# Performance work log

Measured on AMD Instinct MI355X. Metric: run time of the kernel, lower is better.

## Reference

```python
import jax, jax.numpy as jnp
import numpy as np

CH = 64
SCALE = 2
GROUPS = 4
K = 3
GN_GROUPS = min(CH // 8, 8)  # = 8
EPS_GN = 1e-5
EPS_COS = 1e-8


def setup_inputs() -> dict:
    key = jax.random.key(0)
    ks = jax.random.split(key, 4)
    B, H, W = 8, 256, 256
    OC = 2 * GROUPS
    lap = jnp.array([[0., -1., 0.], [-1., 4., -1.], [0., -1., 0.]], dtype=jnp.float32)
    hp_weight = jnp.tile(lap[None, None], (CH, 1, 1, 1))  # depthwise high-pass kernel
    return {
        "x": jax.random.normal(ks[0], (B, CH, H, W), dtype=jnp.float32),
        "gn_gamma": jnp.ones((CH,), jnp.float32),
        "gn_beta": jnp.zeros((CH,), jnp.float32),
        "hp_weight": hp_weight,
        "dir_w": jax.random.normal(ks[1], (OC, K * K - 1), jnp.float32) * 0.001,
        "dir_b": jnp.zeros((OC,), jnp.float32),
        "mag_w": jax.random.normal(ks[2], (OC, CH), jnp.float32) * 0.02,
        "mag_b": jnp.zeros((OC,), jnp.float32),
        "hfg_w": jax.random.normal(ks[3], (OC, CH), jnp.float32) * 0.02,
        "hfg_b": jnp.zeros((OC,), jnp.float32),
    }


def group_norm(x, gamma, beta, g, eps=EPS_GN):
    B, C, H, W = x.shape
    xr = x.reshape(B, g, -1)
    mu = xr.mean(-1, keepdims=True)
    var = xr.var(-1, keepdims=True)
    xn = ((xr - mu) * jax.lax.rsqrt(var + eps)).reshape(B, C, H, W)
    return xn * gamma[None, :, None, None] + beta[None, :, None, None]


def dw_conv3(x, w):
    # depthwise 3x3, padding=1, no bias
    return jax.lax.conv_general_dilated(
        x, w, window_strides=(1, 1), padding=((1, 1), (1, 1)),
        dimension_numbers=("NCHW", "OIHW", "NCHW"), feature_group_count=x.shape[1])


def avg_pool(x, s):
    B, C, H, W = x.shape
    return x.reshape(B, C, H // s, s, W // s, s).mean(axis=(3, 5))


def direction_feat(x, k=K):
    # cosine similarity (over channels) of center pixel vs each of k*k neighbors, center dropped
    B, C, H, W = x.shape
    p = k // 2
    xp = jnp.pad(x, ((0, 0), (0, 0), (p, p), (p, p)))
    patches = jnp.stack([xp[:, :, i:i + H, j:j + W]
                         for i in range(k) for j in range(k)], axis=2)  # [B,C,k2,H,W]
    center = patches[:, :, k * k // 2:k * k // 2 + 1]  # [B,C,1,H,W]
    dot = (center * patches).sum(axis=1)               # [B,k2,H,W]
    n1 = jnp.sqrt((center * center).sum(axis=1))       # [B,1,H,W]
    n2 = jnp.sqrt((patches * patches).sum(axis=1))     # [B,k2,H,W]
    sim = dot / (jnp.maximum(n1, EPS_COS) * jnp.maximum(n2, EPS_COS))
    c = k * k // 2
    return jnp.concatenate([sim[:, :c], sim[:, c + 1:]], axis=1)  # [B,k2-1,H,W]


def conv1x1(w, b, x):
    return jnp.einsum("oc,bchw->bohw", w, x) + b[None, :, None, None]


def grid_sample_border(x, grid):
    # x: [N,C,H,W]; grid: [N,Hg,Wg,2] in [-1,1]; bilinear, align_corners=False, padding_mode='border'
    N, C, H, W = x.shape
    gx, gy = grid[..., 0], grid[..., 1]
    ix = jnp.clip(((gx + 1.0) * W - 1.0) * 0.5, 0.0, W - 1.0)
    iy = jnp.clip(((gy + 1.0) * H - 1.0) * 0.5, 0.0, H - 1.0)
    x0 = jnp.floor(ix); y0 = jnp.floor(iy)
    wx = (ix - x0)[..., None]; wy = (iy - y0)[..., None]
    x0i = jnp.clip(x0.astype(jnp.int32), 0, W - 1)
    y0i = jnp.clip(y0.astype(jnp.int32), 0, H - 1)
    x1i = jnp.clip(x0i + 1, 0, W - 1)
    y1i = jnp.clip(y0i + 1, 0, H - 1)
    img = x.transpose(0, 2, 3, 1)  # [N,H,W,C]
    b = jnp.arange(N)[:, None, None]
    v00 = img[b, y0i, x0i]; v01 = img[b, y0i, x1i]
    v10 = img[b, y1i, x0i]; v11 = img[b, y1i, x1i]
    out = (v00 * (1 - wx) * (1 - wy) + v01 * wx * (1 - wy)
           + v10 * (1 - wx) * wy + v11 * wx * wy)
    return out.transpose(0, 3, 1, 2)  # [N,C,Hg,Wg]


def reference(x, gn_gamma, gn_beta, hp_weight, dir_w, dir_b, mag_w, mag_b, hfg_w, hfg_b):
    B, C, H, W = x.shape
    xn = group_norm(x, gn_gamma, gn_beta, GN_GROUPS)
    hf = dw_conv3(xn, hp_weight)
    xl = avg_pool(xn, SCALE)
    hfl = avg_pool(hf, SCALE)
    df = direction_feat(xl)
    gate = jax.nn.sigmoid(conv1x1(mag_w, mag_b, xl) + conv1x1(hfg_w, hfg_b, hfl))
    offset = conv1x1(dir_w, dir_b, df) * gate  # [B, 2*GROUPS, Hl, Wl]
    Hl, Wl = H // SCALE, W // SCALE
    off = offset.reshape(B, 2, GROUPS, Hl, Wl)
    cy = jnp.arange(Hl, dtype=x.dtype) * SCALE + SCALE / 2.0  # high-res pixel centers
    cx = jnp.arange(Wl, dtype=x.dtype) * SCALE + SCALE / 2.0
    gx = (cx[None, None, None, :] + off[:, 0]) * (2.0 / W) - 1.0  # [B,G,Hl,Wl]
    gy = (cy[None, None, :, None] + off[:, 1]) * (2.0 / H) - 1.0
    grid = jnp.stack([gx, gy], axis=-1).reshape(B * GROUPS, Hl, Wl, 2)
    xg = x.reshape(B * GROUPS, C // GROUPS, H, W)
    out = grid_sample_border(xg, grid)
    return out.reshape(B, C, Hl, Wl)
```

## Files before the change

### kernel.cpp

```cpp
#include <hip/hip_runtime.h>
#include <hip/hip_bf16.h>
#include <math.h>

#define B_ 8
#define C_ 64
#define H_ 256
#define W_ 256
#define HL_ 128
#define WL_ 128
#define GN_G 8
#define CPG 8
#define GRP 4
#define OC_ 8
#define GROUP_ELEMS (CPG * H_ * W_)

#define TILE_H 16
#define XROWS 34
#define EOW 132

__global__ __launch_bounds__(256) void k2_fused(const float* __restrict__ x,
                                                const float* __restrict__ hpw,
                                                float* __restrict__ px,
                                                float* __restrict__ pL,
                                                float* __restrict__ partials) {
  __shared__ float E[XROWS][EOW];
  __shared__ float O[XROWS][EOW];
  __shared__ float rs[4], rs2[4];
  const int t = threadIdx.x;
  const int blk = blockIdx.x;
  const int tileIdx = blk & 7;
  const int bc = blk >> 3;
  const int c = bc & 63;
  const int hl0 = tileIdx * TILE_H;
  const float* plane = x + (size_t)bc * (H_ * W_);
  const int y0 = 2 * hl0 - 1;

  if (t < XROWS * 2) {
    const int r = t >> 1;
    if (t & 1) E[r][128] = 0.f; else O[r][0] = 0.f;
  }

  float s = 0.f, s2 = 0.f;
  for (int i = 0; i < 9; ++i) {
    const int q = t + i * 256;
    if (q >= XROWS * 64) break;
    const int r = q >> 6;
    const int k = q & 63;
    const int y = y0 + r;
    float4 v = make_float4(0.f, 0.f, 0.f, 0.f);
    if ((unsigned)y < (unsigned)H_)
      v = *reinterpret_cast<const float4*>(plane + y * W_ + (k << 2));
    E[r][2 * k]     = v.x;
    E[r][2 * k + 1] = v.z;
    O[r][2 * k + 1] = v.y;
    O[r][2 * k + 2] = v.w;
    if (r >= 1 && r <= 32) {
      s  += v.x + v.y + v.z + v.w;
      s2 += v.x * v.x + v.y * v.y + v.z * v.z + v.w * v.w;
    }
  }
#pragma unroll
  for (int off = 32; off > 0; off >>= 1) {
    s  += __shfl_down(s, off, 64);
    s2 += __shfl_down(s2, off, 64);
  }
  if ((t & 63) == 0) { rs[t >> 6] = s; rs2[t >> 6] = s2; }
  __syncthreads();
  if (t == 0) {
    partials[blk * 2 + 0] = rs[0] + rs[1] + rs[2] + rs[3];
    partials[blk * 2 + 1] = rs2[0] + rs2[1] + rs2[2] + rs2[3];
  }

  float w[9];
#pragma unroll
  for (int i = 0; i < 9; ++i) w[i] = hpw[c * 9 + i];

  const int wl = t & 127;
  const int hs = (t >> 7) * 8;
  const int rbase = 2 * hs;
  float win[4][4];
#pragma unroll
  for (int j = 0; j < 4; ++j) {
    win[j][0] = O[rbase + j][wl];
    win[j][1] = E[rbase + j][wl];
    win[j][2] = O[rbase + j][wl + 1];
    win[j][3] = E[rbase + j][wl + 1];
  }

  int outIdx = (bc * HL_ + (hl0 + hs)) * WL_ + wl;
#pragma unroll
  for (int i = 0; i < 8; ++i) {
    float pr[4][3];
#pragma unroll
    for (int j = 0; j < 4; ++j)
#pragma unroll
      for (int d = 0; d < 3; ++d) pr[j][d] = win[j][d] + win[j][d + 1];
    float hfsum = 0.f;
    float q11 = 0.f;
#pragma unroll
    for (int j = 0; j < 3; ++j)
#pragma unroll
      for (int d = 0; d < 3; ++d) {
        const float qq = pr[j][d] + pr[j + 1][d];
        hfsum = fmaf(w[j * 3 + d], qq, hfsum);
        if (j == 1 && d == 1) q11 = qq;
      }
    px[outIdx] = 0.25f * q11;
    pL[outIdx] = 0.25f * hfsum;
    outIdx += WL_;
    if (i < 7) {
      const int rn = rbase + 2 * i + 4;
#pragma unroll
      for (int d = 0; d < 4; ++d) {
        win[0][d] = win[2][d];
        win[1][d] = win[3][d];
      }
      win[2][0] = O[rn][wl];     win[2][1] = E[rn][wl];
      win[2][2] = O[rn][wl + 1]; win[2][3] = E[rn][wl + 1];
      win[3][0] = O[rn + 1][wl];     win[3][1] = E[rn + 1][wl];
      win[3][2] = O[rn + 1][wl + 1]; win[3][3] = E[rn + 1][wl + 1];
    }
  }
}

__global__ __launch_bounds__(512) void k1_finish(const float* __restrict__ partials,
                                                 const float* __restrict__ gamma,
                                                 const float* __restrict__ beta,
                                                 float* __restrict__ ab) {
  const int t = threadIdx.x;
  const int b = t >> 6, c = t & 63, g = c >> 3;
  float S = 0.f, S2 = 0.f;
  for (int c2 = g * CPG; c2 < g * CPG + CPG; ++c2)
#pragma unroll
    for (int p = 0; p < 8; ++p) {
      const int blk = (b * 64 + c2) * 8 + p;
      S  += partials[blk * 2 + 0];
      S2 += partials[blk * 2 + 1];
    }
  const float N = (float)GROUP_ELEMS;
  const float mean = S / N;
  const float var = fmaxf(S2 / N - mean * mean, 0.f);
  const float a = rsqrtf(var + 1e-5f) * gamma[c];
  ab[t * 2 + 0] = a;
  ab[t * 2 + 1] = beta[c] - mean * a;
}

#define TS 16
__global__ __launch_bounds__(256) void k3_offset(const float* __restrict__ px,
                                                 const float* __restrict__ pL,
                                                 const float* __restrict__ ab,
                                                 const float* __restrict__ dir_w,
                                                 const float* __restrict__ dir_b,
                                                 const float* __restrict__ mag_w,
                                                 const float* __restrict__ mag_b,
                                                 const float* __restrict__ hfg_w,
                                                 const float* __restrict__ hfg_b,
                                                 float2* __restrict__ grid) {
  __shared__ float s_v[2][16][18][24];
  __shared__ float s_mw[C_][OC_];
  __shared__ float s_hw[C_][OC_];
  __shared__ float s_dir[OC_][8];
  __shared__ float s_ab2[C_][2];
  __shared__ float s_bias[2][OC_];

  const int tid = threadIdx.x;
  const int bx = blockIdx.x;
  const int tx = bx & 7, ty = (bx >> 3) & 7, b = bx >> 6;
  const int hl0 = ty * TS, wl0 = tx * TS;
  const size_t planeSz = (size_t)HL_ * WL_;

  for (int i = tid; i < OC_ * C_; i += 256) {
    const int o = i >> 6, c = i & 63;
    s_mw[c][o] = mag_w[i];
    s_hw[c][o] = hfg_w[i];
  }
  if (tid < 64) s_dir[tid >> 3][tid & 7] = dir_w[tid];
  if (tid < 128) s_ab2[tid >> 1][tid & 1] = ab[b * 128 + tid];
  if (tid < OC_) { s_bias[0][tid] = mag_b[tid] + hfg_b[tid]; s_bias[1][tid] = dir_b[tid]; }
  __syncthreads();

  auto stage = [&](int cc, int sel) {
    for (int q = tid; q < 16 * 18 * 6; q += 256) {
      const int c = q / 108, rem = q % 108, r = rem / 6, f4 = rem % 6;
      const int cg = cc * 16 + c;
      const int gy = hl0 - 1 + r;
      const int gx0 = wl0 - 4 + f4 * 4;
      const float a = s_ab2[cg][0], bb = s_ab2[cg][1];
      const float* pp = px + (size_t)(b * C_ + cg) * planeSz + gy * WL_ + gx0;
      float4 v = make_float4(0.f, 0.f, 0.f, 0.f);
      if ((unsigned)gy < (unsigned)HL_) {
        if (gx0 >= 0 && gx0 + 3 < WL_) {
          v = *reinterpret_cast<const float4*>(pp);
          v.x = fmaf(a, v.x, bb); v.y = fmaf(a, v.y, bb);
          v.z = fmaf(a, v.z, bb); v.w = fmaf(a, v.w, bb);
        } else {
          if ((unsigned)(gx0 + 0) < (unsigned)WL_) v.x = fmaf(a, pp[0], bb);
          if ((unsigned)(gx0 + 1) < (unsigned)WL_) v.y = fmaf(a, pp[1], bb);
          if ((unsigned)(gx0 + 2) < (unsigned)WL_) v.z = fmaf(a, pp[2], bb);
          if ((unsigned)(gx0 + 3) < (unsigned)WL_) v.w = fmaf(a, pp[3], bb);
        }
      }
      *reinterpret_cast<float4*>(&s_v[sel][c][r][f4 * 4]) = v;
    }
  };

  const int pxi = tid & 15, pyi = tid >> 4;
  const int hl = hl0 + pyi, wl = wl0 + pxi;
  const float mterm = 0.5f * ((hl == 0) + (hl == HL_ - 1) + (wl == 0) + (wl == WL_ - 1));

  float dot[8], n2[8], z[8], n1 = 0.f;
#pragma unroll
  for (int k = 0; k < 8; ++k) { dot[k] = 0.f; n2[k] = 0.f; z[k] = 0.f; }

  stage(0, 0);
  __syncthreads();

  for (int cc = 0; cc < 4; ++cc) {
    if (cc < 3) stage(cc + 1, (cc + 1) & 1);
    const int sel = cc & 1;
    float lh[16];
    const size_t pbase = (size_t)(b * C_ + cc * 16) * planeSz + hl * WL_ + wl;
#pragma unroll
    for (int c = 0; c < 16; ++c) lh[c] = pL[pbase + c * planeSz];
#pragma unroll
    for (int c = 0; c < 16; ++c) {
      const int cg = cc * 16 + c;
      const float a = s_ab2[cg][0], bb = s_ab2[cg][1];
      const float vc = s_v[sel][c][pyi + 1][pxi + 4];
      const float vh = fmaf(a, lh[c], bb * mterm);
      n1 = fmaf(vc, vc, n1);
      const float u0 = s_v[sel][c][pyi][pxi + 3];
      const float u1 = s_v[sel][c][pyi][pxi + 4];
      const float u2 = s_v[sel][c][pyi][pxi + 5];
      const float u3 = s_v[sel][c][pyi + 1][pxi + 3];
      const float u4 = s_v[sel][c][pyi + 1][pxi + 5];
      const float u5 = s_v[sel][c][pyi + 2][pxi + 3];
      const float u6 = s_v[sel][c][pyi + 2][pxi + 4];
      const float u7 = s_v[sel][c][pyi + 2][pxi + 5];
      dot[0] = fmaf(vc, u0, dot[0]); n2[0] = fmaf(u0, u0, n2[0]);
      dot[1] = fmaf(vc, u1, dot[1]); n2[1] = fmaf(u1, u1, n2[1]);
      dot[2] = fmaf(vc, u2, dot[2]); n2[2] = fmaf(u2, u2, n2[2]);
      dot[3] = fmaf(vc, u3, dot[3]); n2[3] = fmaf(u3, u3, n2[3]);
      dot[4] = fmaf(vc, u4, dot[4]); n2[4] = fmaf(u4, u4, n2[4]);
      dot[5] = fmaf(vc, u5, dot[5]); n2[5] = fmaf(u5, u5, n2[5]);
      dot[6] = fmaf(vc, u6, dot[6]); n2[6] = fmaf(u6, u6, n2[6]);
      dot[7] = fmaf(vc, u7, dot[7]); n2[7] = fmaf(u7, u7, n2[7]);
      const float4 mw0 = *reinterpret_cast<const float4*>(&s_mw[cg][0]);
      const float4 mw1 = *reinterpret_cast<const float4*>(&s_mw[cg][4]);
      const float4 hw0 = *reinterpret_cast<const float4*>(&s_hw[cg][0]);
      const float4 hw1 = *reinterpret_cast<const float4*>(&s_hw[cg][4]);
      z[0] = fmaf(mw0.x, vc, fmaf(hw0.x, vh, z[0]));
      z[1] = fmaf(mw0.y, vc, fmaf(hw0.y, vh, z[1]));
      z[2] = fmaf(mw0.z, vc, fmaf(hw0.z, vh, z[2]));
      z[3] = fmaf(mw0.w, vc, fmaf(hw0.w, vh, z[3]));
      z[4] = fmaf(mw1.x, vc, fmaf(hw1.x, vh, z[4]));
      z[5] = fmaf(mw1.y, vc, fmaf(hw1.y, vh, z[5]));
      z[6] = fmaf(mw1.z, vc, fmaf(hw1.z, vh, z[6]));
      z[7] = fmaf(mw1.w, vc, fmaf(hw1.w, vh, z[7]));
    }
    __syncthreads();
  }

  const float n1c = fmaxf(sqrtf(n1), 1e-8f);
  float df[8];
#pragma unroll
  for (int k = 0; k < 8; ++k)
    df[k] = dot[k] / (n1c * fmaxf(sqrtf(n2[k]), 1e-8f));

  float off[8];
#pragma unroll
  for (int o = 0; o < 8; ++o) {
    float t1 = s_bias[1][o];
#pragma unroll
    for (int j = 0; j < 8; ++j) t1 = fmaf(s_dir[o][j], df[j], t1);
    const float zz = z[o] + s_bias[0][o];
    off[o] = t1 / (1.f + expf(-zz));
  }

#pragma unroll
  for (int g = 0; g < GRP; ++g) {
    const float ix = fminf(fmaxf(2.f * wl + 0.5f + off[g], 0.f), (float)(W_ - 1));
    const float iy = fminf(fmaxf(2.f * hl + 0.5f + off[GRP + g], 0.f), (float)(H_ - 1));
    grid[(b * GRP + g) * (HL_ * WL_) + hl * WL_ + wl] = make_float2(ix, iy);
  }
}

__global__ __launch_bounds__(256) void k4_sample(const float* __restrict__ x,
                                                 const float2* __restrict__ grid,
                                                 float* __restrict__ out) {
  const int idx = blockIdx.x * 256 + threadIdx.x;
  const int wl = idx & (WL_ - 1);
  const int hl = (idx >> 7) & (HL_ - 1);
  const int qc = (idx >> 14) & 3;
  const int g = (idx >> 16) & 3;
  const int b = idx >> 18;
  const float2 G = grid[(b * GRP + g) * (HL_ * WL_) + hl * WL_ + wl];
  const float x0f = floorf(G.x), y0f = floorf(G.y);
  const float wx = G.x - x0f, wy = G.y - y0f;
  const int x0 = (int)x0f, y0 = (int)y0f;
  const float w00 = (1.f - wx) * (1.f - wy), w01 = wx * (1.f - wy);
  const float w10 = (1.f - wx) * wy,        w11 = wx * wy;
  const int c0 = g * 16 + qc * 4;
  const float* plane = x + (size_t)(b * C_ + c0) * (H_ * W_);
  float* po = out + (size_t)(b * C_ + c0) * (HL_ * WL_) + hl * WL_ + wl;

  if (__builtin_expect(((x0 | y0) & 1) == 0, 1)) {
#pragma unroll
    for (int j = 0; j < 4; ++j) {
      const float2 r0 = *reinterpret_cast<const float2*>(plane + y0 * W_ + x0);
      const float2 r1 = *reinterpret_cast<const float2*>(plane + (y0 + 1) * W_ + x0);
      *po = fmaf(r0.x, w00, fmaf(r0.y, w01, fmaf(r1.x, w10, r1.y * w11)));
      plane += H_ * W_;
      po += HL_ * WL_;
    }
  } else {
    const int x1 = min(x0 + 1, W_ - 1), y1 = min(y0 + 1, H_ - 1);
#pragma unroll
    for (int j = 0; j < 4; ++j) {
      const float v00 = plane[y0 * W_ + x0];
      const float v01 = plane[y0 * W_ + x1];
      const float v10 = plane[y1 * W_ + x0];
      const float v11 = plane[y1 * W_ + x1];
      *po = fmaf(v00, w00, fmaf(v01, w01, fmaf(v10, w10, v11 * w11)));
      plane += H_ * W_;
      po += HL_ * WL_;
    }
  }
}

extern "C" void kernel_launch(void* const* d_in, const int* in_sizes, int n_in,
                              void* d_out, int out_size, void* d_ws, size_t ws_size,
                              hipStream_t stream) {
  const float* x = (const float*)d_in[0];
  const float* gn_gamma = (const float*)d_in[1];
  const float* gn_beta = (const float*)d_in[2];
  const float* hp_weight = (const float*)d_in[3];
  const float* dir_w = (const float*)d_in[4];
  const float* dir_b = (const float*)d_in[5];
  const float* mag_w = (const float*)d_in[6];
  const float* mag_b = (const float*)d_in[7];
  const float* hfg_w = (const float*)d_in[8];
  const float* hfg_b = (const float*)d_in[9];
  float* out = (float*)d_out;

  float* ws = (float*)d_ws;
  float* partials = ws;
  float* ab = ws + 8192;
  float* px = ws + 16384;
  float* pL = px + (size_t)B_ * C_ * HL_ * WL_;
  float2* grid = (float2*)(pL + (size_t)B_ * C_ * HL_ * WL_);

  k2_fused<<<B_ * C_ * 8, 256, 0, stream>>>(x, hp_weight, px, pL, partials);
  k1_finish<<<1, 512, 0, stream>>>(partials, gn_gamma, gn_beta, ab);
  k3_offset<<<B_ * (HL_ / TS) * (WL_ / TS), 256, 0, stream>>>(px, pL, ab, dir_w, dir_b,
                                                              mag_w, mag_b, hfg_w, hfg_b, grid);
  k4_sample<<<(B_ * GRP * 4 * HL_ * WL_) / 256, 256, 0, stream>>>(x, grid, out);
}
```

Baseline: 103.8 us.

## Fuse offset computation with grid sampling into a single kernel

```diff
diff --git a/kernel.cpp b/kernel.cpp
--- a/kernel.cpp
+++ b/kernel.cpp
@@ -146,7 +146,8 @@
 }
 
 #define TS 16
-__global__ __launch_bounds__(256) void k3_offset(const float* __restrict__ px,
+__global__ __launch_bounds__(256) void k34_fused(const float* __restrict__ x,
+                                                 const float* __restrict__ px,
                                                  const float* __restrict__ pL,
                                                  const float* __restrict__ ab,
                                                  const float* __restrict__ dir_w,
@@ -155,7 +156,7 @@
                                                  const float* __restrict__ mag_b,
                                                  const float* __restrict__ hfg_w,
                                                  const float* __restrict__ hfg_b,
-                                                 float2* __restrict__ grid) {
+                                                 float* __restrict__ out) {
   __shared__ float s_v[2][16][18][24];
   __shared__ float s_mw[C_][OC_];
   __shared__ float s_hw[C_][OC_];
@@ -277,53 +278,40 @@
     off[o] = t1 / (1.f + expf(-zz));
   }
 
+  const float* planeB = x + (size_t)(b * C_) * (H_ * W_);
+  float* outB = out + (size_t)(b * C_) * planeSz + hl * WL_ + wl;
 #pragma unroll
   for (int g = 0; g < GRP; ++g) {
     const float ix = fminf(fmaxf(2.f * wl + 0.5f + off[g], 0.f), (float)(W_ - 1));
     const float iy = fminf(fmaxf(2.f * hl + 0.5f + off[GRP + g], 0.f), (float)(H_ - 1));
-    grid[(b * GRP + g) * (HL_ * WL_) + hl * WL_ + wl] = make_float2(ix, iy);
-  }
-}
-
-__global__ __launch_bounds__(256) void k4_sample(const float* __restrict__ x,
-                                                 const float2* __restrict__ grid,
-                                                 float* __restrict__ out) {
-  const int idx = blockIdx.x * 256 + threadIdx.x;
-  const int wl = idx & (WL_ - 1);
-  const int hl = (idx >> 7) & (HL_ - 1);
-  const int qc = (idx >> 14) & 3;
-  const int g = (idx >> 16) & 3;
-  const int b = idx >> 18;
-  const float2 G = grid[(b * GRP + g) * (HL_ * WL_) + hl * WL_ + wl];
-  const float x0f = floorf(G.x), y0f = floorf(G.y);
-  const float wx = G.x - x0f, wy = G.y - y0f;
-  const int x0 = (int)x0f, y0 = (int)y0f;
-  const float w00 = (1.f - wx) * (1.f - wy), w01 = wx * (1.f - wy);
-  const float w10 = (1.f - wx) * wy,        w11 = wx * wy;
-  const int c0 = g * 16 + qc * 4;
-  const float* plane = x + (size_t)(b * C_ + c0) * (H_ * W_);
-  float* po = out + (size_t)(b * C_ + c0) * (HL_ * WL_) + hl * WL_ + wl;
-
-  if (__builtin_expect(((x0 | y0) & 1) == 0, 1)) {
-#pragma unroll
-    for (int j = 0; j < 4; ++j) {
-      const float2 r0 = *reinterpret_cast<const float2*>(plane + y0 * W_ + x0);
-      const float2 r1 = *reinterpret_cast<const float2*>(plane + (y0 + 1) * W_ + x0);
-      *po = fmaf(r0.x, w00, fmaf(r0.y, w01, fmaf(r1.x, w10, r1.y * w11)));
-      plane += H_ * W_;
-      po += HL_ * WL_;
-    }
-  } else {
-    const int x1 = min(x0 + 1, W_ - 1), y1 = min(y0 + 1, H_ - 1);
-#pragma unroll
-    for (int j = 0; j < 4; ++j) {
-      const float v00 = plane[y0 * W_ + x0];
-      const float v01 = plane[y0 * W_ + x1];
-      const float v10 = plane[y1 * W_ + x0];
-      const float v11 = plane[y1 * W_ + x1];
-      *po = fmaf(v00, w00, fmaf(v01, w01, fmaf(v10, w10, v11 * w11)));
-      plane += H_ * W_;
-      po += HL_ * WL_;
+    const float x0f = floorf(ix), y0f = floorf(iy);
+    const float wx = ix - x0f, wy = iy - y0f;
+    const int x0 = (int)x0f, y0 = (int)y0f;
+    const float w00 = (1.f - wx) * (1.f - wy), w01 = wx * (1.f - wy);
+    const float w10 = (1.f - wx) * wy,        w11 = wx * wy;
+    const float* pc = planeB + (size_t)(g * 16) * (H_ * W_);
+    float* oc = outB + (size_t)(g * 16) * planeSz;
+    if (__builtin_expect(((x0 | y0) & 1) == 0, 1)) {
+#pragma unroll 4
+      for (int c2 = 0; c2 < 16; ++c2) {
+        const float2 r0 = *reinterpret_cast<const float2*>(pc + y0 * W_ + x0);
+        const float2 r1 = *reinterpret_cast<const float2*>(pc + (y0 + 1) * W_ + x0);
+        *oc = fmaf(r0.x, w00, fmaf(r0.y, w01, fmaf(r1.x, w10, r1.y * w11)));
+        pc += H_ * W_;
+        oc += planeSz;
+      }
+    } else {
+      const int x1 = min(x0 + 1, W_ - 1), y1 = min(y0 + 1, H_ - 1);
+#pragma unroll 4
+      for (int c2 = 0; c2 < 16; ++c2) {
+        const float v00 = pc[y0 * W_ + x0];
+        const float v01 = pc[y0 * W_ + x1];
+        const float v10 = pc[y1 * W_ + x0];
+        const float v11 = pc[y1 * W_ + x1];
+        *oc = fmaf(v00, w00, fmaf(v01, w01, fmaf(v10, w10, v11 * w11)));
+        pc += H_ * W_;
+        oc += planeSz;
+      }
     }
   }
 }
@@ -348,11 +336,9 @@
   float* ab = ws + 8192;
   float* px = ws + 16384;
   float* pL = px + (size_t)B_ * C_ * HL_ * WL_;
-  float2* grid = (float2*)(pL + (size_t)B_ * C_ * HL_ * WL_);
 
   k2_fused<<<B_ * C_ * 8, 256, 0, stream>>>(x, hp_weight, px, pL, partials);
   k1_finish<<<1, 512, 0, stream>>>(partials, gn_gamma, gn_beta, ab);
-  k3_offset<<<B_ * (HL_ / TS) * (WL_ / TS), 256, 0, stream>>>(px, pL, ab, dir_w, dir_b,
-                                                              mag_w, mag_b, hfg_w, hfg_b, grid);
-  k4_sample<<<(B_ * GRP * 4 * HL_ * WL_) / 256, 256, 0, stream>>>(x, grid, out);
+  k34_fused<<<B_ * (HL_ / TS) * (WL_ / TS), 256, 0, stream>>>(x, px, pL, ab, dir_w, dir_b,
+                                                              mag_w, mag_b, hfg_w, hfg_b, out);
 }
```

Result: faster. 98.19 us (-5.4%).
